# Kernel tuning notes

Hardware: AMD Instinct MI355X
Metric: run time of the kernel (lower is better)

The kernel has to match this reference:

```python
import jax, jax.numpy as jnp
import numpy as np

N, E, M, F, L = 50000, 800000, 50000, 64, 20
HID = 32
NEG_SLOPE = 0.2


def gatv2(x, src, dst, Wl, Wr, att, b, heads, outc):
    # PyG GATv2Conv (eval mode, dropout off), self-loops already in src/dst.
    n = x.shape[0]
    xl = (x @ Wl).reshape(n, heads, outc)
    xr = (x @ Wr).reshape(n, heads, outc)
    e = jax.nn.leaky_relu(xl[src] + xr[dst], NEG_SLOPE)          # [E, H, C]
    score = jnp.einsum('ehc,hc->eh', e, att)                      # [E, H]
    smax = jax.ops.segment_max(score, dst, num_segments=n)
    ex = jnp.exp(score - smax[dst])
    denom = jax.ops.segment_sum(ex, dst, num_segments=n)
    alpha = ex / denom[dst]                                       # scatter-softmax
    out = jax.ops.segment_sum(alpha[:, :, None] * xl[src], dst, num_segments=n)
    return out.reshape(n, heads * outc) + b


def setup_inputs() -> dict:
    key = jax.random.key(0)
    ks = jax.random.split(key, 32)
    d = {}
    d['x'] = jax.random.normal(ks[0], (N, 60), jnp.float32)
    d['lane_x'] = jax.random.normal(ks[1], (M, 2), jnp.float32)
    d['centerline'] = jax.random.normal(ks[2], (F, L, 2), jnp.float32)
    d['edge_index'] = jax.random.randint(ks[3], (2, E), 0, N)
    d['focal_idx'] = jax.random.randint(ks[4], (F,), 0, N)
    s = 0.1
    d['emb_W'] = jax.random.normal(ks[5], (60, HID)) * s
    d['emb_b'] = jnp.zeros((HID,))
    d['c1_Wl'] = jax.random.normal(ks[6], (HID, 4 * HID)) * s
    d['c1_Wr'] = jax.random.normal(ks[7], (HID, 4 * HID)) * s
    d['c1_att'] = jax.random.normal(ks[8], (4, HID)) * s
    d['c1_b'] = jnp.zeros((4 * HID,))
    d['c2_Wl'] = jax.random.normal(ks[9], (4 * HID, 4 * HID)) * s
    d['c2_Wr'] = jax.random.normal(ks[10], (4 * HID, 4 * HID)) * s
    d['c2_att'] = jax.random.normal(ks[11], (4, HID)) * s
    d['c2_b'] = jnp.zeros((4 * HID,))
    d['map_W'] = jax.random.normal(ks[12], (2, HID)) * s
    d['map_b'] = jnp.zeros((HID,))
    d['gg_Wl'] = jax.random.normal(ks[13], (4 * HID, HID)) * s
    d['gg_Wr'] = jax.random.normal(ks[14], (4 * HID, HID)) * s
    d['gg_att'] = jax.random.normal(ks[15], (1, HID)) * s
    d['gg_b'] = jnp.zeros((HID,))
    d['cl_W'] = jax.random.normal(ks[16], (2, HID)) * s
    d['cl_b'] = jnp.zeros((HID,))
    d['fc1_W'] = jax.random.normal(ks[17], (3 * HID, HID)) * s
    d['fc1_b'] = jnp.zeros((HID,))
    d['fc2_W'] = jax.random.normal(ks[18], (HID, HID // 2)) * s
    d['fc2_b'] = jnp.zeros((HID // 2,))
    d['fco_W'] = jax.random.normal(ks[19], (HID // 2, 60)) * s
    d['fco_b'] = jnp.zeros((60,))
    return d


def reference(x, lane_x, centerline, edge_index, focal_idx,
              emb_W, emb_b, c1_Wl, c1_Wr, c1_att, c1_b,
              c2_Wl, c2_Wr, c2_att, c2_b, map_W, map_b,
              gg_Wl, gg_Wr, gg_att, gg_b, cl_W, cl_b,
              fc1_W, fc1_b, fc2_W, fc2_b, fco_W, fco_b):
    n = x.shape[0]
    loops = jnp.arange(n)
    src = jnp.concatenate([edge_index[0], loops])  # PyG adds self-loops
    dst = jnp.concatenate([edge_index[1], loops])
    # agent encoder + subgraph (two GATv2 layers, heads=4, concat)
    h = jax.nn.relu(x @ emb_W + emb_b)                                   # [N,32]
    h = jax.nn.relu(gatv2(h, src, dst, c1_Wl, c1_Wr, c1_att, c1_b, 4, HID))
    agent_feat = jax.nn.relu(gatv2(h, src, dst, c2_Wl, c2_Wr, c2_att, c2_b, 4, HID))  # [N,128]
    # map branch (executable path: no lane edges -> plain embedding + mean pool)
    map_x = jax.nn.relu(lane_x @ map_W + map_b)                          # [M,32]
    map_global = jnp.mean(map_x, axis=0, keepdims=True)                  # [1,32]
    # global graph (heads=1)
    gf = jax.nn.relu(gatv2(agent_feat, src, dst, gg_Wl, gg_Wr, gg_att, gg_b, 1, HID))  # [N,32]
    focal = gf[focal_idx]                                                # [F,32]
    map_g = jnp.broadcast_to(map_global, (focal.shape[0], HID))
    cl = jnp.mean(centerline, axis=1) @ cl_W + cl_b                      # [F,32]
    comb = jnp.concatenate([focal, map_g, cl], axis=1)                   # [F,96]
    h = jax.nn.relu(comb @ fc1_W + fc1_b)
    h = jax.nn.relu(h @ fc2_W + fc2_b)
    return h @ fco_W + fco_b                                             # [F,60]
```

## Files before the change

### kernel.cpp

```cpp
#include <hip/hip_runtime.h>
#include <hip/hip_bf16.h>
#include <hip/hip_fp16.h>

typedef _Float16 half_t;
typedef _Float16 h8 __attribute__((ext_vector_type(8)));
typedef _Float16 h4v __attribute__((ext_vector_type(4)));
typedef _Float16 h2v __attribute__((ext_vector_type(2)));
typedef float f4v __attribute__((ext_vector_type(4)));

union H8u { h8 v; h2v h2[4]; _Float16 e[8]; };
union H4u { h4v v; h2v h2[2]; _Float16 e[4]; };

static inline int cdiv(long a, long b) { return (int)((a + b - 1) / b); }

__device__ __forceinline__ void fma4(float4& a, float s, const float4& w) {
    a.x += s * w.x; a.y += s * w.y; a.z += s * w.z; a.w += s * w.w;
}

__device__ __forceinline__ h8 hmax8(h8 a, h8 b) {
#if __has_builtin(__builtin_elementwise_max)
    return __builtin_elementwise_max(a, b);
#else
    h8 r;
#pragma unroll
    for (int j = 0; j < 8; ++j) r[j] = (a[j] > b[j]) ? a[j] : b[j];
    return r;
#endif
}
__device__ __forceinline__ h4v hmax4(h4v a, h4v b) {
#if __has_builtin(__builtin_elementwise_max)
    return __builtin_elementwise_max(a, b);
#else
    h4v r;
#pragma unroll
    for (int j = 0; j < 4; ++j) r[j] = (a[j] > b[j]) ? a[j] : b[j];
    return r;
#endif
}

__device__ __forceinline__ float dot2acc(h2v a, h2v b, float c) {
#if __has_builtin(__builtin_amdgcn_fdot2)
    return __builtin_amdgcn_fdot2(a, b, c, false);
#else
    return c + (float)a.x * (float)b.x + (float)a.y * (float)b.y;
#endif
}


template <int K4, int C4, int R>
__global__ __launch_bounds__(256) void gemm_t_h(
        const float* __restrict__ X, const float* __restrict__ W,
        const float* __restrict__ bias, half_t* __restrict__ Y,
        int Nr, int relu) {
    int idx = blockIdx.x * blockDim.x + threadIdx.x;
    int total = (Nr / R) * C4;
    if (idx >= total) return;
    int c4 = idx % C4;
    int n0 = (idx / C4) * R;
    const float4* __restrict__ Wv = (const float4*)W;
    const float4* __restrict__ Xv = (const float4*)X;
    float4 acc[R];
    float4 binit = bias ? ((const float4*)bias)[c4] : make_float4(0.f, 0.f, 0.f, 0.f);
#pragma unroll
    for (int r = 0; r < R; ++r) acc[r] = binit;
#pragma unroll 4
    for (int k4 = 0; k4 < K4; ++k4) {
        float4 w0 = Wv[(size_t)(4 * k4 + 0) * C4 + c4];
        float4 w1 = Wv[(size_t)(4 * k4 + 1) * C4 + c4];
        float4 w2 = Wv[(size_t)(4 * k4 + 2) * C4 + c4];
        float4 w3 = Wv[(size_t)(4 * k4 + 3) * C4 + c4];
#pragma unroll
        for (int r = 0; r < R; ++r) {
            float4 xv = Xv[(size_t)(n0 + r) * K4 + k4];
            fma4(acc[r], xv.x, w0); fma4(acc[r], xv.y, w1);
            fma4(acc[r], xv.z, w2); fma4(acc[r], xv.w, w3);
        }
    }
#pragma unroll
    for (int r = 0; r < R; ++r) {
        float4 o = acc[r];
        if (relu) {
            o.x = fmaxf(o.x, 0.f); o.y = fmaxf(o.y, 0.f);
            o.z = fmaxf(o.z, 0.f); o.w = fmaxf(o.w, 0.f);
        }
        h4v oh; oh.x = (half_t)o.x; oh.y = (half_t)o.y; oh.z = (half_t)o.z; oh.w = (half_t)o.w;
        ((h4v*)Y)[(size_t)(n0 + r) * C4 + c4] = oh;
    }
}


__global__ void wtrans(const float* __restrict__ c1l, const float* __restrict__ c1r,
                       const float* __restrict__ c2l, const float* __restrict__ c2r,
                       const float* __restrict__ ggl, const float* __restrict__ ggr,
                       const float* __restrict__ at1, const float* __restrict__ at2,
                       const float* __restrict__ atg, half_t* __restrict__ dst) {
    int idx = blockIdx.x * blockDim.x + threadIdx.x;
    if (idx >= 49440) return;
    if (idx >= 49152) {
        int j = idx - 49152;
        float v = (j < 128) ? at1[j] : (j < 256) ? at2[j - 128] : atg[j - 256];
        dst[idx] = (half_t)v;
        return;
    }
    const float* src; int K, loc;
    if (idx < 8192) {
        K = 32;
        if (idx < 4096) { src = c1l; loc = idx; } else { src = c1r; loc = idx - 4096; }
        int k = loc % K, c = loc / K;
        dst[idx] = (half_t)src[k * 128 + c];
    } else if (idx < 40960) {
        K = 128;
        if (idx < 24576) { src = c2l; loc = idx - 8192; } else { src = c2r; loc = idx - 24576; }
        int k = loc % K, c = loc / K;
        dst[idx] = (half_t)src[k * 128 + c];
    } else {
        K = 128;
        if (idx < 45056) { src = ggl; loc = idx - 40960; } else { src = ggr; loc = idx - 45056; }
        int k = loc % K, c = loc / K;
        dst[idx] = (half_t)src[k * 32 + c];
    }
}


template <int K, int C1>
__global__ __launch_bounds__(256) void mfma_dual(
        const half_t* __restrict__ Xh,
        const half_t* __restrict__ W1t, const half_t* __restrict__ W2t,
        half_t* __restrict__ Y1, half_t* __restrict__ Y2, int Nr) {
    constexpr int KT = K / 32;
    constexpr int NBC = (2 * C1) / 64;
    int wave = threadIdx.x >> 6, lane = threadIdx.x & 63;
    int bCol = blockIdx.x % NBC;
    int bRow = blockIdx.x / NBC;
    int rowBase = bRow * 128 + wave * 32;
    int colBase = bCol * 64;
    int m = lane & 15, quad = lane >> 4;

    f4v acc[2][4] = {};

    const half_t* bptr[4];
#pragma unroll
    for (int nt = 0; nt < 4; ++nt) {
        int gc = colBase + nt * 16 + m;
        bptr[nt] = (gc < C1) ? (W1t + (size_t)gc * K) : (W2t + (size_t)(gc - C1) * K);
    }
    int r0 = rowBase + m, r1 = rowBase + 16 + m;
    int r0c = (r0 < Nr) ? r0 : (Nr - 1);
    int r1c = (r1 < Nr) ? r1 : (Nr - 1);
    const half_t* a0p = Xh + (size_t)r0c * K + quad * 8;
    const half_t* a1p = Xh + (size_t)r1c * K + quad * 8;

#pragma unroll
    for (int kk = 0; kk < KT; ++kk) {
        h8 a0 = *(const h8*)(a0p + kk * 32);
        h8 a1 = *(const h8*)(a1p + kk * 32);
#pragma unroll
        for (int nt = 0; nt < 4; ++nt) {
            h8 b = *(const h8*)(bptr[nt] + kk * 32 + quad * 8);
            acc[0][nt] = __builtin_amdgcn_mfma_f32_16x16x32_f16(a0, b, acc[0][nt], 0, 0, 0);
            acc[1][nt] = __builtin_amdgcn_mfma_f32_16x16x32_f16(a1, b, acc[1][nt], 0, 0, 0);
        }
    }

#pragma unroll
    for (int mt = 0; mt < 2; ++mt) {
#pragma unroll
        for (int nt = 0; nt < 4; ++nt) {
            int gc = colBase + nt * 16 + m;
            half_t* Y = (gc < C1) ? (Y1 + gc) : (Y2 + (gc - C1));
#pragma unroll
            for (int r = 0; r < 4; ++r) {
                int gr = rowBase + mt * 16 + quad * 4 + r;
                if (gr < Nr) Y[(size_t)gr * C1] = (half_t)acc[mt][nt][r];
            }
        }
    }
}


__global__ void count_dst(const int* __restrict__ ei, int* __restrict__ counts, int E) {
    int e = blockIdx.x * blockDim.x + threadIdx.x;
    if (e >= E) return;
    atomicAdd(&counts[ei[E + e]], 1);
}

#define SCAN_CH 2048

__global__ void reduce_chunks(const int* __restrict__ counts, int* __restrict__ partial, int N) {
    __shared__ int sh[256];
    int t = threadIdx.x, base = blockIdx.x * SCAN_CH + t * 8;
    int s = 0;
    for (int j = 0; j < 8; ++j) if (base + j < N) s += counts[base + j] + 1;
    sh[t] = s; __syncthreads();
    for (int off = 128; off >= 1; off >>= 1) {
        if (t < off) sh[t] += sh[t + off];
        __syncthreads();
    }
    if (t == 0) partial[blockIdx.x] = sh[0];
}

__global__ void scan_partials(int* __restrict__ partial, int nch) {
    if (threadIdx.x == 0 && blockIdx.x == 0) {
        int run = 0;
        for (int i = 0; i < nch; ++i) { int v = partial[i]; partial[i] = run; run += v; }
    }
}

__global__ void scan_chunks(int* __restrict__ counts, const int* __restrict__ partial,
                            int* __restrict__ offsets, int* __restrict__ cursor,
                            int* __restrict__ adj, int N) {
    __shared__ int sh[256];
    int t = threadIdx.x, b = blockIdx.x, base = b * SCAN_CH + t * 8;
    int v[8], s = 0;
    for (int j = 0; j < 8; ++j) {
        v[j] = (base + j < N) ? (counts[base + j] + 1) : 0;
        s += v[j];
    }
    sh[t] = s; __syncthreads();
    for (int off = 1; off < 256; off <<= 1) {
        int x = (t >= off) ? sh[t - off] : 0;
        __syncthreads();
        sh[t] += x;
        __syncthreads();
    }
    int run = partial[b] + (t == 0 ? 0 : sh[t - 1]);
    for (int j = 0; j < 8; ++j) {
        if (base + j < N) {
            offsets[base + j] = run;
            adj[run] = base + j;
            cursor[base + j] = run + 1;
            counts[base + j] = v[j];
        }
        run += v[j];
    }
}

__global__ __launch_bounds__(256) void fill_adj_sliced(
        const int* __restrict__ ei, int* __restrict__ cursor,
        int* __restrict__ adj, int E, int sliceSz) {
    int slice = blockIdx.x & 7;
    int lo = slice * sliceSz, hi = lo + sliceSz;
    int nb = gridDim.x >> 3;
    int bi = blockIdx.x >> 3;
    int stride = nb * 256;
    for (int e = bi * 256 + threadIdx.x; e < E; e += stride) {
        int d = ei[E + e];
        if (d >= lo && d < hi) {
            int pos = atomicAdd(&cursor[d], 1);
            adj[pos] = ei[e];
        }
    }
}

__global__ __launch_bounds__(256) void sort_adj(
        const int* __restrict__ offsets, const int* __restrict__ counts,
        int* __restrict__ adj, int N) {
    int wave = threadIdx.x >> 6, lane = threadIdx.x & 63;
    int d = blockIdx.x * 4 + wave;
    if (d >= N) return;
    int off = offsets[d];
    int deg = counts[d];
    int m = (deg < 64) ? deg : 64;
    int v = (lane < m) ? adj[off + lane] : 0x7fffffff;
#pragma unroll 4
    for (int r = 0; r < 64; ++r) {
        int p;
        if ((r & 1) == 0) p = lane ^ 1;
        else p = (lane == 0 || lane == 63) ? lane : ((lane & 1) ? lane + 1 : lane - 1);
        int pv = __shfl(v, p);
        v = (lane < p) ? ((v < pv) ? v : pv) : ((lane > p) ? ((v > pv) ? v : pv) : v);
    }
    if (lane < m) adj[off + lane] = v;
}


__global__ __launch_bounds__(256) void gat16_h4(
        const half_t* __restrict__ xl, const half_t* __restrict__ xr,
        const half_t* __restrict__ atth, const int* __restrict__ offsets,
        const int* __restrict__ counts, const int* __restrict__ adj,
        const float* __restrict__ bias, half_t* __restrict__ out, int N) {
    int wave = threadIdx.x >> 6, lane = threadIdx.x & 63;
    int g = lane >> 4, t = lane & 15;
    int d = blockIdx.x * 16 + wave * 4 + g;
    int dc = (d < N) ? d : (N - 1);
    int off = offsets[dc];
    int deg = (d < N) ? counts[dc] : 0;
    int dmax = deg;
    dmax = max(dmax, __shfl_xor(dmax, 16));
    dmax = max(dmax, __shfl_xor(dmax, 32));

    h8 xr8 = *(const h8*)(xr + (size_t)dc * 128 + t * 8);
    H8u at8; at8.v = *(const h8*)(atth + t * 8);

    float acc[8];
#pragma unroll
    for (int j = 0; j < 8; ++j) acc[j] = 0.f;
    float lsum = 0.f;
    h8 c02;
#pragma unroll
    for (int j = 0; j < 8; ++j) c02[j] = (half_t)0.2f;

    bool v0 = 0 < deg, v1 = 1 < deg, v2 = 2 < deg, v3 = 3 < deg;
    int s0 = adj[off];
    int s1 = adj[off + (v1 ? 1 : 0)];
    int s2 = adj[off + (v2 ? 2 : 0)];
    int s3 = adj[off + (v3 ? 3 : 0)];

    for (int i = 0; i < dmax; i += 4) {
        H8u a0, a1, a2, a3;
        a0.v = *(const h8*)(xl + (size_t)s0 * 128 + t * 8);
        a1.v = *(const h8*)(xl + (size_t)s1 * 128 + t * 8);
        a2.v = *(const h8*)(xl + (size_t)s2 * 128 + t * 8);
        a3.v = *(const h8*)(xl + (size_t)s3 * 128 + t * 8);
        int ni = i + 4;
        bool nv0 = ni < deg, nv1 = ni + 1 < deg, nv2 = ni + 2 < deg, nv3 = ni + 3 < deg;
        int n0 = adj[off + (nv0 ? ni : 0)];
        int n1 = adj[off + (nv1 ? ni + 1 : 0)];
        int n2 = adj[off + (nv2 ? ni + 2 : 0)];
        int n3 = adj[off + (nv3 ? ni + 3 : 0)];

        h8 e0 = a0.v + xr8, e1 = a1.v + xr8, e2 = a2.v + xr8, e3 = a3.v + xr8;
        H8u l0, l1, l2, l3;
        l0.v = hmax8(e0, e0 * c02);
        l1.v = hmax8(e1, e1 * c02);
        l2.v = hmax8(e2, e2 * c02);
        l3.v = hmax8(e3, e3 * c02);
        float p0 = 0.f, p1 = 0.f, p2 = 0.f, p3 = 0.f;
#pragma unroll
        for (int j = 0; j < 4; ++j) {
            p0 = dot2acc(l0.h2[j], at8.h2[j], p0);
            p1 = dot2acc(l1.h2[j], at8.h2[j], p1);
            p2 = dot2acc(l2.h2[j], at8.h2[j], p2);
            p3 = dot2acc(l3.h2[j], at8.h2[j], p3);
        }
        p0 += __shfl_xor(p0, 1); p1 += __shfl_xor(p1, 1);
        p2 += __shfl_xor(p2, 1); p3 += __shfl_xor(p3, 1);
        p0 += __shfl_xor(p0, 2); p1 += __shfl_xor(p1, 2);
        p2 += __shfl_xor(p2, 2); p3 += __shfl_xor(p3, 2);
        float w0 = v0 ? __expf(p0) : 0.f;
        float w1 = v1 ? __expf(p1) : 0.f;
        float w2 = v2 ? __expf(p2) : 0.f;
        float w3 = v3 ? __expf(p3) : 0.f;
        lsum += (w0 + w1) + (w2 + w3);
#pragma unroll
        for (int j = 0; j < 8; ++j)
            acc[j] += w0 * (float)a0.e[j] + w1 * (float)a1.e[j]
                    + w2 * (float)a2.e[j] + w3 * (float)a3.e[j];
        s0 = n0; s1 = n1; s2 = n2; s3 = n3;
        v0 = nv0; v1 = nv1; v2 = nv2; v3 = nv3;
    }

    if (d < N) {
        float inv = 1.f / lsum;
        H8u o;
#pragma unroll
        for (int j = 0; j < 8; ++j)
            o.e[j] = (half_t)fmaxf(acc[j] * inv + bias[t * 8 + j], 0.f);
        *(h8*)(out + (size_t)d * 128 + t * 8) = o.v;
    }
}

__global__ __launch_bounds__(256) void gat16_h1(
        const half_t* __restrict__ xl, const half_t* __restrict__ xr,
        const half_t* __restrict__ atth, const int* __restrict__ offsets,
        const int* __restrict__ counts, const int* __restrict__ adj,
        const float* __restrict__ bias, float* __restrict__ out, int N) {
    int wave = threadIdx.x >> 6, lane = threadIdx.x & 63;
    int g = lane >> 4, sub = (lane >> 3) & 1, t = lane & 7;
    int d = blockIdx.x * 16 + wave * 4 + g;
    int dc = (d < N) ? d : (N - 1);
    int off = offsets[dc];
    int deg = (d < N) ? counts[dc] : 0;
    int dmax = deg;
    dmax = max(dmax, __shfl_xor(dmax, 16));
    dmax = max(dmax, __shfl_xor(dmax, 32));

    h4v xr4 = *(const h4v*)(xr + (size_t)dc * 32 + t * 4);
    H4u at4; at4.v = *(const h4v*)(atth + t * 4);

    float acc[4] = {0.f, 0.f, 0.f, 0.f};
    float lsum = 0.f;
    h4v c02;
#pragma unroll
    for (int j = 0; j < 4; ++j) c02[j] = (half_t)0.2f;

    int i = sub;
    bool va = i < deg, vb = i + 2 < deg, vc = i + 4 < deg, vd = i + 6 < deg;
    int sa = adj[off + (va ? i : 0)];
    int sb = adj[off + (vb ? i + 2 : 0)];
    int sc = adj[off + (vc ? i + 4 : 0)];
    int sd = adj[off + (vd ? i + 6 : 0)];
    for (; i < dmax; i += 8) {
        H4u a, b, c, e;
        a.v = *(const h4v*)(xl + (size_t)sa * 32 + t * 4);
        b.v = *(const h4v*)(xl + (size_t)sb * 32 + t * 4);
        c.v = *(const h4v*)(xl + (size_t)sc * 32 + t * 4);
        e.v = *(const h4v*)(xl + (size_t)sd * 32 + t * 4);
        int ni = i + 8;
        bool nva = ni < deg, nvb = ni + 2 < deg, nvc = ni + 4 < deg, nvd = ni + 6 < deg;
        int na = adj[off + (nva ? ni : 0)];
        int nb = adj[off + (nvb ? ni + 2 : 0)];
        int nc = adj[off + (nvc ? ni + 4 : 0)];
        int nd = adj[off + (nvd ? ni + 6 : 0)];
        h4v ea = a.v + xr4, eb = b.v + xr4, ec = c.v + xr4, ed = e.v + xr4;
        H4u la, lb, lc, ld;
        la.v = hmax4(ea, ea * c02);
        lb.v = hmax4(eb, eb * c02);
        lc.v = hmax4(ec, ec * c02);
        ld.v = hmax4(ed, ed * c02);
        float pa = dot2acc(la.h2[0], at4.h2[0], 0.f);
        float pb = dot2acc(lb.h2[0], at4.h2[0], 0.f);
        float pc = dot2acc(lc.h2[0], at4.h2[0], 0.f);
        float pd = dot2acc(ld.h2[0], at4.h2[0], 0.f);
        pa = dot2acc(la.h2[1], at4.h2[1], pa);
        pb = dot2acc(lb.h2[1], at4.h2[1], pb);
        pc = dot2acc(lc.h2[1], at4.h2[1], pc);
        pd = dot2acc(ld.h2[1], at4.h2[1], pd);
        pa += __shfl_xor(pa, 1); pb += __shfl_xor(pb, 1);
        pc += __shfl_xor(pc, 1); pd += __shfl_xor(pd, 1);
        pa += __shfl_xor(pa, 2); pb += __shfl_xor(pb, 2);
        pc += __shfl_xor(pc, 2); pd += __shfl_xor(pd, 2);
        pa += __shfl_xor(pa, 4); pb += __shfl_xor(pb, 4);
        pc += __shfl_xor(pc, 4); pd += __shfl_xor(pd, 4);
        float wa = va ? __expf(pa) : 0.f;
        float wb = vb ? __expf(pb) : 0.f;
        float wc = vc ? __expf(pc) : 0.f;
        float wd = vd ? __expf(pd) : 0.f;
        lsum += (wa + wb) + (wc + wd);
#pragma unroll
        for (int j = 0; j < 4; ++j)
            acc[j] += wa * (float)a.e[j] + wb * (float)b.e[j]
                    + wc * (float)c.e[j] + wd * (float)e.e[j];
        sa = na; sb = nb; sc = nc; sd = nd;
        va = nva; vb = nvb; vc = nvc; vd = nvd;
    }

    lsum += __shfl_xor(lsum, 8);
#pragma unroll
    for (int j = 0; j < 4; ++j) acc[j] += __shfl_xor(acc[j], 8);

    if (d < N && sub == 0) {
        float inv = 1.f / lsum;
        float4 o;
        o.x = fmaxf(acc[0] * inv + bias[t * 4 + 0], 0.f);
        o.y = fmaxf(acc[1] * inv + bias[t * 4 + 1], 0.f);
        o.z = fmaxf(acc[2] * inv + bias[t * 4 + 2], 0.f);
        o.w = fmaxf(acc[3] * inv + bias[t * 4 + 3], 0.f);
        *(float4*)(out + (size_t)d * 32 + t * 4) = o;
    }
}


__global__ void map_sum_kernel(const float* __restrict__ lane_x, const float* __restrict__ map_W,
                               const float* __restrict__ map_b, float* __restrict__ sums, int M) {
    __shared__ float s[32];
    if (threadIdx.x < 32) s[threadIdx.x] = 0.f;
    __syncthreads();
    int t = blockIdx.x * blockDim.x + threadIdx.x;
    int nth = gridDim.x * blockDim.x;
    int c = t & 31;
    float w0 = map_W[c], w1 = map_W[32 + c], bb = map_b[c];
    float acc = 0.f;
    for (int m = t >> 5; m < M; m += nth >> 5) {
        float v = lane_x[(long)m * 2] * w0 + lane_x[(long)m * 2 + 1] * w1 + bb;
        acc += fmaxf(v, 0.f);
    }
    atomicAdd(&s[c], acc);
    __syncthreads();
    if (threadIdx.x < 32) atomicAdd(&sums[threadIdx.x], s[threadIdx.x]);
}


__global__ void head_kernel(const float* __restrict__ gf, const int* __restrict__ focal_idx,
                            const float* __restrict__ map_sums, int M,
                            const float* __restrict__ centerline, int L,
                            const float* __restrict__ cl_W, const float* __restrict__ cl_b,
                            const float* __restrict__ fc1_W, const float* __restrict__ fc1_b,
                            const float* __restrict__ fc2_W, const float* __restrict__ fc2_b,
                            const float* __restrict__ fco_W, const float* __restrict__ fco_b,
                            float* __restrict__ out) {
    int f = blockIdx.x;
    int lane = threadIdx.x;
    __shared__ float s_comb[96];
    __shared__ float s_h1[32];
    __shared__ float s_h2[16];
    __shared__ float s_cl[2];

    float c0 = 0.f, c1 = 0.f;
    if (lane < L) {
        c0 = centerline[((long)f * L + lane) * 2 + 0];
        c1 = centerline[((long)f * L + lane) * 2 + 1];
    }
    for (int off = 32; off >= 1; off >>= 1) {
        c0 += __shfl_down(c0, off);
        c1 += __shfl_down(c1, off);
    }
    if (lane == 0) { s_cl[0] = c0 / (float)L; s_cl[1] = c1 / (float)L; }
    __syncthreads();

    int fi = focal_idx[f];
    if (lane < 32) {
        s_comb[lane] = gf[(long)fi * 32 + lane];
        s_comb[32 + lane] = map_sums[lane] / (float)M;
        s_comb[64 + lane] = s_cl[0] * cl_W[lane] + s_cl[1] * cl_W[32 + lane] + cl_b[lane];
    }
    __syncthreads();

    if (lane < 32) {
        float acc = fc1_b[lane];
        for (int k = 0; k < 96; ++k) acc += s_comb[k] * fc1_W[k * 32 + lane];
        s_h1[lane] = fmaxf(acc, 0.f);
    }
    __syncthreads();

    if (lane < 16) {
        float acc = fc2_b[lane];
        for (int k = 0; k < 32; ++k) acc += s_h1[k] * fc2_W[k * 16 + lane];
        s_h2[lane] = fmaxf(acc, 0.f);
    }
    __syncthreads();

    if (lane < 60) {
        float acc = fco_b[lane];
        for (int k = 0; k < 16; ++k) acc += s_h2[k] * fco_W[k * 60 + lane];
        out[(long)f * 60 + lane] = acc;
    }
}


extern "C" void kernel_launch(void* const* d_in, const int* in_sizes, int n_in,
                              void* d_out, int out_size, void* d_ws, size_t ws_size,
                              hipStream_t stream) {
    const float* x          = (const float*)d_in[0];
    const float* lane_x     = (const float*)d_in[1];
    const float* centerline = (const float*)d_in[2];
    const int*   ei         = (const int*)d_in[3];
    const int*   focal_idx  = (const int*)d_in[4];
    const float* emb_W = (const float*)d_in[5];
    const float* emb_b = (const float*)d_in[6];
    const float* c1_Wl = (const float*)d_in[7];
    const float* c1_Wr = (const float*)d_in[8];
    const float* c1_att = (const float*)d_in[9];
    const float* c1_b  = (const float*)d_in[10];
    const float* c2_Wl = (const float*)d_in[11];
    const float* c2_Wr = (const float*)d_in[12];
    const float* c2_att = (const float*)d_in[13];
    const float* c2_b  = (const float*)d_in[14];
    const float* map_W = (const float*)d_in[15];
    const float* map_b = (const float*)d_in[16];
    const float* gg_Wl = (const float*)d_in[17];
    const float* gg_Wr = (const float*)d_in[18];
    const float* gg_att = (const float*)d_in[19];
    const float* gg_b  = (const float*)d_in[20];
    const float* cl_W  = (const float*)d_in[21];
    const float* cl_b  = (const float*)d_in[22];
    const float* fc1_W = (const float*)d_in[23];
    const float* fc1_b = (const float*)d_in[24];
    const float* fc2_W = (const float*)d_in[25];
    const float* fc2_b = (const float*)d_in[26];
    const float* fco_W = (const float*)d_in[27];
    const float* fco_b = (const float*)d_in[28];

    const int N = in_sizes[0] / 60;
    const int M = in_sizes[1] / 2;
    const int F = in_sizes[4];
    const int L = in_sizes[2] / (F * 2);
    const int E = in_sizes[3] / 2;
    const int Etot = E + N;

    half_t* Xl_h = (half_t*)d_ws;
    half_t* Xr_h = Xl_h + (size_t)N * 128;
    half_t* H0_h = Xr_h + (size_t)N * 128;
    half_t* H1_h = H0_h + (size_t)N * 32;
    half_t* AF_h = H1_h + (size_t)N * 128;
    float*  GF_f = (float*)(AF_h + (size_t)N * 128);
    half_t* Wt   = (half_t*)(GF_f + (size_t)N * 32);
    int* counts  = (int*)(Wt + 49440);
    int* offsets = counts + N;
    int* cursor  = offsets + N;
    int* adj     = cursor + N;
    float* MAPS  = (float*)(adj + Etot);
    int* partial = (int*)(MAPS + 32);

    half_t* c1Wlt = Wt + 0;
    half_t* c1Wrt = Wt + 4096;
    half_t* c2Wlt = Wt + 8192;
    half_t* c2Wrt = Wt + 24576;
    half_t* ggWlt = Wt + 40960;
    half_t* ggWrt = Wt + 45056;
    half_t* att1h = Wt + 49152;
    half_t* att2h = Wt + 49280;
    half_t* attgh = Wt + 49408;

    const int BS = 256;
    const int nch = cdiv(N, SCAN_CH);
    const int rowBlocks = cdiv(N, 128);
    const int sliceSz = cdiv(N, 8);

    hipMemsetAsync(counts, 0, (size_t)N * sizeof(int), stream);
    count_dst<<<cdiv(E, BS), BS, 0, stream>>>(ei, counts, E);
    reduce_chunks<<<nch, 256, 0, stream>>>(counts, partial, N);
    scan_partials<<<1, 64, 0, stream>>>(partial, nch);
    scan_chunks<<<nch, 256, 0, stream>>>(counts, partial, offsets, cursor, adj, N);
    fill_adj_sliced<<<8 * 104, 256, 0, stream>>>(ei, cursor, adj, E, sliceSz);
    sort_adj<<<cdiv(N, 4), 256, 0, stream>>>(offsets, counts, adj, N);

    wtrans<<<cdiv(49440, BS), BS, 0, stream>>>(c1_Wl, c1_Wr, c2_Wl, c2_Wr, gg_Wl, gg_Wr,
                                               c1_att, c2_att, gg_att, Wt);

    gemm_t_h<15, 8, 4><<<cdiv((long)(N / 4) * 8, BS), BS, 0, stream>>>(x, emb_W, emb_b, H0_h, N, 1);

    mfma_dual<32, 128><<<rowBlocks * 4, 256, 0, stream>>>(H0_h, c1Wlt, c1Wrt, Xl_h, Xr_h, N);
    gat16_h4<<<cdiv(N, 16), 256, 0, stream>>>(Xl_h, Xr_h, att1h, offsets, counts, adj, c1_b, H1_h, N);

    mfma_dual<128, 128><<<rowBlocks * 4, 256, 0, stream>>>(H1_h, c2Wlt, c2Wrt, Xl_h, Xr_h, N);
    gat16_h4<<<cdiv(N, 16), 256, 0, stream>>>(Xl_h, Xr_h, att2h, offsets, counts, adj, c2_b, AF_h, N);

    mfma_dual<128, 32><<<rowBlocks * 1, 256, 0, stream>>>(AF_h, ggWlt, ggWrt, Xl_h, Xr_h, N);
    gat16_h1<<<cdiv(N, 16), 256, 0, stream>>>(Xl_h, Xr_h, attgh, offsets, counts, adj, gg_b, GF_f, N);

    hipMemsetAsync(MAPS, 0, 32 * sizeof(float), stream);
    map_sum_kernel<<<64, BS, 0, stream>>>(lane_x, map_W, map_b, MAPS, M);

    head_kernel<<<F, 64, 0, stream>>>(GF_f, focal_idx, MAPS, M, centerline, L,
                                      cl_W, cl_b, fc1_W, fc1_b, fc2_W, fc2_b,
                                      fco_W, fco_b, (float*)d_out);
}
```

Baseline: 418.7 us.

## Replace per-node adjacency sort with 8-bucket source binning in CSR build

Builds the CSR with a count per (destination, source-bucket) pair using 8 buckets over source index ranges. The fill step then scatters edges, self-loops included, into bucket order, and the bitonic-style sort_adj kernel is removed. The aim is to drop the sort pass while keeping neighbor gathers roughly grouped by source locality for cache reuse. In exchange the count, scan and offset arrays grow eightfold and the scan does more work. Order within a bucket is no longer deterministic.

```diff
diff --git a/kernel.cpp b/kernel.cpp
--- a/kernel.cpp
+++ b/kernel.cpp
@@ -178,19 +178,26 @@
 }
 
 
-__global__ void count_dst(const int* __restrict__ ei, int* __restrict__ counts, int E) {
+#define NBKT 8
+#define BSH 13
+
+__global__ void count_dst8(const int* __restrict__ ei, int* __restrict__ counts8,
+                           int E, int N) {
     int e = blockIdx.x * blockDim.x + threadIdx.x;
-    if (e >= E) return;
-    atomicAdd(&counts[ei[E + e]], 1);
+    if (e >= E + N) return;
+    int d, s;
+    if (e < E) { d = ei[E + e]; s = ei[e]; }
+    else { d = e - E; s = d; }
+    atomicAdd(&counts8[(size_t)d * NBKT + (s >> BSH)], 1);
 }
 
 #define SCAN_CH 2048
 
-__global__ void reduce_chunks(const int* __restrict__ counts, int* __restrict__ partial, int N) {
+__global__ void reduce_chunks(const int* __restrict__ counts8, int* __restrict__ partial, int n8) {
     __shared__ int sh[256];
     int t = threadIdx.x, base = blockIdx.x * SCAN_CH + t * 8;
     int s = 0;
-    for (int j = 0; j < 8; ++j) if (base + j < N) s += counts[base + j] + 1;
+    for (int j = 0; j < 8; ++j) if (base + j < n8) s += counts8[base + j];
     sh[t] = s; __syncthreads();
     for (int off = 128; off >= 1; off >>= 1) {
         if (t < off) sh[t] += sh[t + off];
@@ -206,14 +213,13 @@
     }
 }
 
-__global__ void scan_chunks(int* __restrict__ counts, const int* __restrict__ partial,
-                            int* __restrict__ offsets, int* __restrict__ cursor,
-                            int* __restrict__ adj, int N) {
+__global__ void scan_chunks(const int* __restrict__ counts8, const int* __restrict__ partial,
+                            int* __restrict__ offsets8, int* __restrict__ cursor8, int n8) {
     __shared__ int sh[256];
     int t = threadIdx.x, b = blockIdx.x, base = b * SCAN_CH + t * 8;
     int v[8], s = 0;
     for (int j = 0; j < 8; ++j) {
-        v[j] = (base + j < N) ? (counts[base + j] + 1) : 0;
+        v[j] = (base + j < n8) ? counts8[base + j] : 0;
         s += v[j];
     }
     sh[t] = s; __syncthreads();
@@ -225,66 +231,47 @@
     }
     int run = partial[b] + (t == 0 ? 0 : sh[t - 1]);
     for (int j = 0; j < 8; ++j) {
-        if (base + j < N) {
-            offsets[base + j] = run;
-            adj[run] = base + j;
-            cursor[base + j] = run + 1;
-            counts[base + j] = v[j];
+        if (base + j < n8) {
+            offsets8[base + j] = run;
+            cursor8[base + j] = run;
         }
         run += v[j];
     }
 }
 
 __global__ __launch_bounds__(256) void fill_adj_sliced(
-        const int* __restrict__ ei, int* __restrict__ cursor,
-        int* __restrict__ adj, int E, int sliceSz) {
+        const int* __restrict__ ei, int* __restrict__ cursor8,
+        int* __restrict__ adj, int E, int N, int sliceSz) {
     int slice = blockIdx.x & 7;
     int lo = slice * sliceSz, hi = lo + sliceSz;
     int nb = gridDim.x >> 3;
     int bi = blockIdx.x >> 3;
     int stride = nb * 256;
-    for (int e = bi * 256 + threadIdx.x; e < E; e += stride) {
-        int d = ei[E + e];
+    int Etot = E + N;
+    for (int e = bi * 256 + threadIdx.x; e < Etot; e += stride) {
+        int d, s;
+        if (e < E) { d = ei[E + e]; s = ei[e]; }
+        else { d = e - E; s = d; }
         if (d >= lo && d < hi) {
-            int pos = atomicAdd(&cursor[d], 1);
-            adj[pos] = ei[e];
+            int pos = atomicAdd(&cursor8[(size_t)d * NBKT + (s >> BSH)], 1);
+            adj[pos] = s;
         }
     }
-}
-
-__global__ __launch_bounds__(256) void sort_adj(
-        const int* __restrict__ offsets, const int* __restrict__ counts,
-        int* __restrict__ adj, int N) {
-    int wave = threadIdx.x >> 6, lane = threadIdx.x & 63;
-    int d = blockIdx.x * 4 + wave;
-    if (d >= N) return;
-    int off = offsets[d];
-    int deg = counts[d];
-    int m = (deg < 64) ? deg : 64;
-    int v = (lane < m) ? adj[off + lane] : 0x7fffffff;
-#pragma unroll 4
-    for (int r = 0; r < 64; ++r) {
-        int p;
-        if ((r & 1) == 0) p = lane ^ 1;
-        else p = (lane == 0 || lane == 63) ? lane : ((lane & 1) ? lane + 1 : lane - 1);
-        int pv = __shfl(v, p);
-        v = (lane < p) ? ((v < pv) ? v : pv) : ((lane > p) ? ((v > pv) ? v : pv) : v);
-    }
-    if (lane < m) adj[off + lane] = v;
 }
 
 
 __global__ __launch_bounds__(256) void gat16_h4(
         const half_t* __restrict__ xl, const half_t* __restrict__ xr,
-        const half_t* __restrict__ atth, const int* __restrict__ offsets,
-        const int* __restrict__ counts, const int* __restrict__ adj,
-        const float* __restrict__ bias, half_t* __restrict__ out, int N) {
+        const half_t* __restrict__ atth, const int* __restrict__ offsets8,
+        const int* __restrict__ adj,
+        const float* __restrict__ bias, half_t* __restrict__ out, int N, int Etot) {
     int wave = threadIdx.x >> 6, lane = threadIdx.x & 63;
     int g = lane >> 4, t = lane & 15;
     int d = blockIdx.x * 16 + wave * 4 + g;
     int dc = (d < N) ? d : (N - 1);
-    int off = offsets[dc];
-    int deg = (d < N) ? counts[dc] : 0;
+    int off = offsets8[(size_t)dc * NBKT];
+    int nxt = (dc < N - 1) ? offsets8[(size_t)(dc + 1) * NBKT] : Etot;
+    int deg = (d < N) ? (nxt - off) : 0;
     int dmax = deg;
     dmax = max(dmax, __shfl_xor(dmax, 16));
     dmax = max(dmax, __shfl_xor(dmax, 32));
@@ -362,15 +349,16 @@
 
 __global__ __launch_bounds__(256) void gat16_h1(
         const half_t* __restrict__ xl, const half_t* __restrict__ xr,
-        const half_t* __restrict__ atth, const int* __restrict__ offsets,
-        const int* __restrict__ counts, const int* __restrict__ adj,
-        const float* __restrict__ bias, float* __restrict__ out, int N) {
+        const half_t* __restrict__ atth, const int* __restrict__ offsets8,
+        const int* __restrict__ adj,
+        const float* __restrict__ bias, float* __restrict__ out, int N, int Etot) {
     int wave = threadIdx.x >> 6, lane = threadIdx.x & 63;
     int g = lane >> 4, sub = (lane >> 3) & 1, t = lane & 7;
     int d = blockIdx.x * 16 + wave * 4 + g;
     int dc = (d < N) ? d : (N - 1);
-    int off = offsets[dc];
-    int deg = (d < N) ? counts[dc] : 0;
+    int off = offsets8[(size_t)dc * NBKT];
+    int nxt = (dc < N - 1) ? offsets8[(size_t)(dc + 1) * NBKT] : Etot;
+    int deg = (d < N) ? (nxt - off) : 0;
     int dmax = deg;
     dmax = max(dmax, __shfl_xor(dmax, 16));
     dmax = max(dmax, __shfl_xor(dmax, 32));
@@ -567,6 +555,7 @@
     const int L = in_sizes[2] / (F * 2);
     const int E = in_sizes[3] / 2;
     const int Etot = E + N;
+    const int n8 = N * NBKT;
 
     half_t* Xl_h = (half_t*)d_ws;
     half_t* Xr_h = Xl_h + (size_t)N * 128;
@@ -575,12 +564,12 @@
     half_t* AF_h = H1_h + (size_t)N * 128;
     float*  GF_f = (float*)(AF_h + (size_t)N * 128);
     half_t* Wt   = (half_t*)(GF_f + (size_t)N * 32);
-    int* counts  = (int*)(Wt + 49440);
-    int* offsets = counts + N;
-    int* cursor  = offsets + N;
-    int* adj     = cursor + N;
-    float* MAPS  = (float*)(adj + Etot);
-    int* partial = (int*)(MAPS + 32);
+    int* counts8  = (int*)(Wt + 49440);
+    int* offsets8 = counts8 + n8;
+    int* cursor8  = offsets8 + n8;
+    int* adj      = cursor8 + n8;
+    float* MAPS   = (float*)(adj + Etot);
+    int* partial  = (int*)(MAPS + 32);
 
     half_t* c1Wlt = Wt + 0;
     half_t* c1Wrt = Wt + 4096;
@@ -593,17 +582,16 @@
     half_t* attgh = Wt + 49408;
 
     const int BS = 256;
-    const int nch = cdiv(N, SCAN_CH);
+    const int nch = cdiv(n8, SCAN_CH);
     const int rowBlocks = cdiv(N, 128);
     const int sliceSz = cdiv(N, 8);
 
-    hipMemsetAsync(counts, 0, (size_t)N * sizeof(int), stream);
-    count_dst<<<cdiv(E, BS), BS, 0, stream>>>(ei, counts, E);
-    reduce_chunks<<<nch, 256, 0, stream>>>(counts, partial, N);
+    hipMemsetAsync(counts8, 0, (size_t)n8 * sizeof(int), stream);
+    count_dst8<<<cdiv(Etot, BS), BS, 0, stream>>>(ei, counts8, E, N);
+    reduce_chunks<<<nch, 256, 0, stream>>>(counts8, partial, n8);
     scan_partials<<<1, 64, 0, stream>>>(partial, nch);
-    scan_chunks<<<nch, 256, 0, stream>>>(counts, partial, offsets, cursor, adj, N);
-    fill_adj_sliced<<<8 * 104, 256, 0, stream>>>(ei, cursor, adj, E, sliceSz);
-    sort_adj<<<cdiv(N, 4), 256, 0, stream>>>(offsets, counts, adj, N);
+    scan_chunks<<<nch, 256, 0, stream>>>(counts8, partial, offsets8, cursor8, n8);
+    fill_adj_sliced<<<8 * 104, 256, 0, stream>>>(ei, cursor8, adj, E, N, sliceSz);
 
     wtrans<<<cdiv(49440, BS), BS, 0, stream>>>(c1_Wl, c1_Wr, c2_Wl, c2_Wr, gg_Wl, gg_Wr,
                                                c1_att, c2_att, gg_att, Wt);
@@ -611,13 +599,13 @@
     gemm_t_h<15, 8, 4><<<cdiv((long)(N / 4) * 8, BS), BS, 0, stream>>>(x, emb_W, emb_b, H0_h, N, 1);
 
     mfma_dual<32, 128><<<rowBlocks * 4, 256, 0, stream>>>(H0_h, c1Wlt, c1Wrt, Xl_h, Xr_h, N);
-    gat16_h4<<<cdiv(N, 16), 256, 0, stream>>>(Xl_h, Xr_h, att1h, offsets, counts, adj, c1_b, H1_h, N);
+    gat16_h4<<<cdiv(N, 16), 256, 0, stream>>>(Xl_h, Xr_h, att1h, offsets8, adj, c1_b, H1_h, N, Etot);
 
     mfma_dual<128, 128><<<rowBlocks * 4, 256, 0, stream>>>(H1_h, c2Wlt, c2Wrt, Xl_h, Xr_h, N);
-    gat16_h4<<<cdiv(N, 16), 256, 0, stream>>>(Xl_h, Xr_h, att2h, offsets, counts, adj, c2_b, AF_h, N);
+    gat16_h4<<<cdiv(N, 16), 256, 0, stream>>>(Xl_h, Xr_h, att2h, offsets8, adj, c2_b, AF_h, N, Etot);
 
     mfma_dual<128, 32><<<rowBlocks * 1, 256, 0, stream>>>(AF_h, ggWlt, ggWrt, Xl_h, Xr_h, N);
-    gat16_h1<<<cdiv(N, 16), 256, 0, stream>>>(Xl_h, Xr_h, attgh, offsets, counts, adj, gg_b, GF_f, N);
+    gat16_h1<<<cdiv(N, 16), 256, 0, stream>>>(Xl_h, Xr_h, attgh, offsets8, adj, gg_b, GF_f, N, Etot);
 
     hipMemsetAsync(MAPS, 0, 32 * sizeof(float), stream);
     map_sum_kernel<<<64, BS, 0, stream>>>(lane_x, map_W, map_b, MAPS, M);
```

After: 391.5 us. 6.5% less time.
